# Kernel optimization log

Measured on AMD Instinct MI355X. Metric: run time of the kernel, lower is better.

The kernel has to match this reference:

```python
import jax, jax.numpy as jnp
import numpy as np

EPS = 1e-10
NUM_RELATION = 4
N_NODES = 50000
N_EDGES = 800000
D_IN = 128
D_H = 256


def rgc_layer(x, src, dst, rel, rel_w, rel_b, loop_w, loop_b):
    # torchdrug RelationalGraphConv: scatter-mean per (node, relation), then
    # linear over concatenated per-relation features + self-loop linear + relu.
    N, d = x.shape
    msg = x[src]                                      # [E, d] gather
    idx = dst * NUM_RELATION + rel                    # [E] bucket per (node, relation)
    num_seg = N * NUM_RELATION
    agg = jax.ops.segment_sum(msg, idx, num_segments=num_seg)            # [N*R, d]
    cnt = jax.ops.segment_sum(jnp.ones((msg.shape[0], 1), x.dtype), idx,
                              num_segments=num_seg)                       # [N*R, 1]
    update = (agg / (cnt + EPS)).reshape(N, NUM_RELATION * d)            # [N, R*d]
    out = update @ rel_w + rel_b + x @ loop_w + loop_b                   # [N, d_out]
    return jax.nn.relu(out)


def highway(x, hp_w, hp_b, ht_w, ht_b):
    proj = jax.nn.relu(x @ hp_w + hp_b)
    gate = jax.nn.sigmoid(x @ ht_w + ht_b)
    return gate * proj + (1.0 - gate) * x


def setup_inputs() -> dict:
    key = jax.random.key(0)
    ks = jax.random.split(key, 16)
    s = 0.02
    inp = {
        "x": jax.random.normal(ks[0], (N_NODES, D_IN), dtype=jnp.float32),
        "src": jax.random.randint(ks[1], (N_EDGES,), 0, N_NODES, dtype=jnp.int32),
        "dst": jax.random.randint(ks[2], (N_EDGES,), 0, N_NODES, dtype=jnp.int32),
        "rel": jax.random.randint(ks[3], (N_EDGES,), 0, NUM_RELATION, dtype=jnp.int32),
        # layer 1: RGC(128->256) + Highway(256)
        "rel_w1": jax.random.normal(ks[4], (NUM_RELATION * D_IN, D_H), dtype=jnp.float32) * s,
        "rel_b1": jnp.zeros((D_H,), jnp.float32),
        "loop_w1": jax.random.normal(ks[5], (D_IN, D_H), dtype=jnp.float32) * s,
        "loop_b1": jnp.zeros((D_H,), jnp.float32),
        "hp_w1": jax.random.normal(ks[6], (D_H, D_H), dtype=jnp.float32) * s,
        "hp_b1": jnp.zeros((D_H,), jnp.float32),
        "ht_w1": jax.random.normal(ks[7], (D_H, D_H), dtype=jnp.float32) * s,
        "ht_b1": jnp.full((D_H,), -2.0, jnp.float32),  # transform.bias.data.fill_(-2.0)
        # layer 2: RGC(256->256) + Highway(256)
        "rel_w2": jax.random.normal(ks[8], (NUM_RELATION * D_H, D_H), dtype=jnp.float32) * s,
        "rel_b2": jnp.zeros((D_H,), jnp.float32),
        "loop_w2": jax.random.normal(ks[9], (D_H, D_H), dtype=jnp.float32) * s,
        "loop_b2": jnp.zeros((D_H,), jnp.float32),
        "hp_w2": jax.random.normal(ks[10], (D_H, D_H), dtype=jnp.float32) * s,
        "hp_b2": jnp.zeros((D_H,), jnp.float32),
        "ht_w2": jax.random.normal(ks[11], (D_H, D_H), dtype=jnp.float32) * s,
        "ht_b2": jnp.full((D_H,), -2.0, jnp.float32),
    }
    return inp


def reference(x, src, dst, rel,
              rel_w1, rel_b1, loop_w1, loop_b1, hp_w1, hp_b1, ht_w1, ht_b1,
              rel_w2, rel_b2, loop_w2, loop_b2, hp_w2, hp_b2, ht_w2, ht_b2):
    h = rgc_layer(x, src, dst, rel, rel_w1, rel_b1, loop_w1, loop_b1)
    h = highway(h, hp_w1, hp_b1, ht_w1, ht_b1)
    h = rgc_layer(h, src, dst, rel, rel_w2, rel_b2, loop_w2, loop_b2)
    h = highway(h, hp_w2, hp_b2, ht_w2, ht_b2)
    return h  # node_feature, shape [N, 256]
```

## Files before the change

kernel.cpp:

```cpp
#include <hip/hip_runtime.h>

typedef __bf16 bf16_t;
typedef __bf16 bf16x8 __attribute__((ext_vector_type(8)));
typedef __bf16 bf16x4 __attribute__((ext_vector_type(4)));
typedef float f32x4 __attribute__((ext_vector_type(4)));
typedef int i32x4 __attribute__((ext_vector_type(4)));

#define BM 64

__device__ __forceinline__ void gload_lds16(const void* g, void* s) {
    __builtin_amdgcn_global_load_lds(
        (const __attribute__((address_space(1))) unsigned int*)g,
        (__attribute__((address_space(3))) unsigned int*)s, 16, 0, 0);
}

__device__ __forceinline__ void chunk_map(int g, int& row, int& kcol) {
    int L = g >> 3;
    int v = (g & 7) ^ (L & 7);
    row  = 2 * L + (v >> 2);
    kcol = (v & 3) << 3;
}

__device__ __forceinline__ int frag_off(int r, int quad) {
    int L = r >> 1;
    return L * 64 + (((((r & 1) << 2) | quad) ^ (L & 7)) << 3);
}

__global__ __launch_bounds__(256, 4) void gemm_k(
    const bf16_t* __restrict__ A, int lda, int M,
    const bf16_t* __restrict__ Bt, int K,
    const float* __restrict__ bias, int relu_flag,
    bf16_t* __restrict__ outb, int ldo, int ocol,
    int NTM)
{
    __shared__ __align__(16) bf16_t As[2][64 * 32];
    __shared__ __align__(16) bf16_t Bs[2][256 * 32];

    const int L   = blockIdx.x;
    const int xcd = L & 7;
    const int sup = L >> 3;
    const int mt  = sup * 8 + xcd;
    if (mt >= NTM) return;
    const int m0 = mt * BM;

    const int tid  = threadIdx.x;
    const int wave = tid >> 6, lane = tid & 63;
    const int wr   = wave >> 1, wc = wave & 1;
    const int lm   = lane & 15, quad = lane >> 4;

    const bf16_t* ag;
    const bf16_t* bg[4];
    {
        int row, kcol; chunk_map(tid, row, kcol);
        int gm = m0 + row; if (gm >= M) gm = M - 1;
        ag = A + (size_t)gm * lda + kcol;
    }
    #pragma unroll
    for (int j = 0; j < 4; j++) {
        int row, kcol; chunk_map(j * 256 + tid, row, kcol);
        bg[j] = Bt + (size_t)row * K + kcol;
    }

    f32x4 acc[2][8] = {};
    const int nt = K >> 5;

    gload_lds16(ag, &As[0][tid * 8]);
    #pragma unroll
    for (int j = 0; j < 4; j++)
        gload_lds16(bg[j], &Bs[0][(j * 256 + tid) * 8]);
    __syncthreads();

    int cur = 0;
    for (int t = 0; t < nt; ++t) {
        if (t + 1 < nt) {
            int k0n = (t + 1) << 5;
            gload_lds16(ag + k0n, &As[cur ^ 1][tid * 8]);
            #pragma unroll
            for (int j = 0; j < 4; j++)
                gload_lds16(bg[j] + k0n, &Bs[cur ^ 1][(j * 256 + tid) * 8]);
        }
        bf16x8 af[2];
        #pragma unroll
        for (int i = 0; i < 2; i++)
            af[i] = *(const bf16x8*)&As[cur][frag_off(wr * 32 + i * 16 + lm, quad)];
        #pragma unroll
        for (int ni = 0; ni < 8; ni++) {
            bf16x8 bfr = *(const bf16x8*)&Bs[cur][frag_off(wc * 128 + ni * 16 + lm, quad)];
            #pragma unroll
            for (int mi = 0; mi < 2; mi++)
                acc[mi][ni] = __builtin_amdgcn_mfma_f32_16x16x32_bf16(
                    af[mi], bfr, acc[mi][ni], 0, 0, 0);
        }
        __syncthreads();
        cur ^= 1;
    }

    #pragma unroll
    for (int mi = 0; mi < 2; mi++) {
        #pragma unroll
        for (int ni = 0; ni < 8; ni++) {
            int col = wc * 128 + ni * 16 + lm;
            float b = bias[col];
            #pragma unroll
            for (int r = 0; r < 4; r++) {
                int row = m0 + wr * 32 + mi * 16 + quad * 4 + r;
                if (row < M) {
                    float v = acc[mi][ni][r] + b;
                    if (relu_flag) v = fmaxf(v, 0.f);
                    outb[(size_t)row * ldo + ocol + col] = (bf16_t)v;
                }
            }
        }
    }
}

__global__ __launch_bounds__(256, 4) void gemm_hw2(
    const bf16_t* __restrict__ A, int M,
    const bf16_t* __restrict__ Bt,
    const float* __restrict__ bias,
    bf16_t* __restrict__ outb, int ldo, int ocol,
    float* __restrict__ outf, int NTM)
{
    __shared__ __align__(16) bf16_t As[2][64 * 32];
    __shared__ __align__(16) bf16_t Bs[2][256 * 32];

    const int L    = blockIdx.x;
    const int xcd  = L & 7;
    const int rest = L >> 3;
    const int nt2  = rest & 1;
    const int sup  = rest >> 1;
    const int mt   = sup * 8 + xcd;
    if (mt >= NTM) return;
    const int m0 = mt * BM;

    const int tid  = threadIdx.x;
    const int wave = tid >> 6, lane = tid & 63;
    const int lm   = lane & 15, quad = lane >> 4;

    const bf16_t* ag;
    const bf16_t* bg[4];
    {
        int row, kcol; chunk_map(tid, row, kcol);
        int gm = m0 + row; if (gm >= M) gm = M - 1;
        ag = A + (size_t)gm * 256 + kcol;
    }
    #pragma unroll
    for (int j = 0; j < 4; j++) {
        int row, kcol; chunk_map(j * 256 + tid, row, kcol);
        int grow = nt2 * 128 + row + ((row >= 128) ? 128 : 0);
        bg[j] = Bt + (size_t)grow * 256 + kcol;
    }

    f32x4 acc[16] = {};
    const int nt = 8;

    gload_lds16(ag, &As[0][tid * 8]);
    #pragma unroll
    for (int j = 0; j < 4; j++)
        gload_lds16(bg[j], &Bs[0][(j * 256 + tid) * 8]);
    __syncthreads();

    int cur = 0;
    for (int t = 0; t < nt; ++t) {
        if (t + 1 < nt) {
            int k0n = (t + 1) << 5;
            gload_lds16(ag + k0n, &As[cur ^ 1][tid * 8]);
            #pragma unroll
            for (int j = 0; j < 4; j++)
                gload_lds16(bg[j] + k0n, &Bs[cur ^ 1][(j * 256 + tid) * 8]);
        }
        bf16x8 af = *(const bf16x8*)&As[cur][frag_off(wave * 16 + lm, quad)];
        #pragma unroll
        for (int ni = 0; ni < 16; ni++) {
            bf16x8 bfr = *(const bf16x8*)&Bs[cur][frag_off(ni * 16 + lm, quad)];
            acc[ni] = __builtin_amdgcn_mfma_f32_16x16x32_bf16(
                af, bfr, acc[ni], 0, 0, 0);
        }
        __syncthreads();
        cur ^= 1;
    }

    #pragma unroll
    for (int ni = 0; ni < 8; ni++) {
        int col = nt2 * 128 + ni * 16 + lm;
        float bp  = bias[col];
        float bg2 = bias[256 + col];
        #pragma unroll
        for (int r = 0; r < 4; r++) {
            int row = m0 + wave * 16 + quad * 4 + r;
            if (row < M) {
                float p = acc[ni][r] + bp;
                float g = acc[ni + 8][r] + bg2;
                float s = 1.0f / (1.0f + __expf(-g));
                float hv = (float)A[(size_t)row * 256 + col];
                float v = s * fmaxf(p, 0.f) + (1.0f - s) * hv;
                if (outf) outf[(size_t)row * 256 + col] = v;
                else      outb[(size_t)row * ldo + ocol + col] = (bf16_t)v;
            }
        }
    }
}

__global__ void prep_all(
    const float* __restrict__ rel_w1, const float* __restrict__ loop_w1,
    const float* __restrict__ rel_w2, const float* __restrict__ loop_w2,
    const float* __restrict__ hp_w1,  const float* __restrict__ ht_w1,
    const float* __restrict__ hp_w2,  const float* __restrict__ ht_w2,
    bf16_t* __restrict__ W1t, bf16_t* __restrict__ W2t,
    bf16_t* __restrict__ Wh1t, bf16_t* __restrict__ Wh2t,
    const float* __restrict__ rb1, const float* __restrict__ lb1,
    const float* __restrict__ rb2, const float* __restrict__ lb2,
    const float* __restrict__ hpb1, const float* __restrict__ htb1,
    const float* __restrict__ hpb2, const float* __restrict__ htb2,
    float* __restrict__ bR1, float* __restrict__ bR2,
    float* __restrict__ bH1, float* __restrict__ bH2,
    const float* __restrict__ x, bf16_t* __restrict__ A1, int N,
    int* __restrict__ cnt, int NSEG, int cvb)
{
    __shared__ float sh[16][256];
    int b = blockIdx.x, tid = threadIdx.x;
    if (b < 184) {
        const float* W; bf16_t* Wt; int ldk, k0, n0, kb;
        if      (b < 32)  { W = rel_w1;  Wt = W1t;  ldk = 640;  k0 = 0;    n0 = 0;   kb = b; }
        else if (b < 40)  { W = loop_w1; Wt = W1t;  ldk = 640;  k0 = 512;  n0 = 0;   kb = b - 32; }
        else if (b < 104) { W = rel_w2;  Wt = W2t;  ldk = 1280; k0 = 0;    n0 = 0;   kb = b - 40; }
        else if (b < 120) { W = loop_w2; Wt = W2t;  ldk = 1280; k0 = 1024; n0 = 0;   kb = b - 104; }
        else if (b < 136) { W = hp_w1;   Wt = Wh1t; ldk = 256;  k0 = 0;    n0 = 0;   kb = b - 120; }
        else if (b < 152) { W = ht_w1;   Wt = Wh1t; ldk = 256;  k0 = 0;    n0 = 256; kb = b - 136; }
        else if (b < 168) { W = hp_w2;   Wt = Wh2t; ldk = 256;  k0 = 0;    n0 = 0;   kb = b - 152; }
        else              { W = ht_w2;   Wt = Wh2t; ldk = 256;  k0 = 0;    n0 = 256; kb = b - 168; }
        int kb16 = kb * 16;
        #pragma unroll
        for (int kk = 0; kk < 16; kk++)
            sh[kk][tid] = W[(size_t)(kb16 + kk) * 256 + tid];
        __syncthreads();
        bf16x8 o0, o1;
        #pragma unroll
        for (int j = 0; j < 8; j++) {
            o0[j] = (bf16_t)sh[j][tid];
            o1[j] = (bf16_t)sh[8 + j][tid];
        }
        bf16_t* p = Wt + (size_t)(n0 + tid) * ldk + k0 + kb16;
        *(bf16x8*)p = o0;
        *(bf16x8*)(p + 8) = o1;
    } else if (b == 184) {
        int t = tid;
        bR1[t] = rb1[t] + lb1[t];
        bR2[t] = rb2[t] + lb2[t];
        bH1[t] = hpb1[t]; bH1[256 + t] = htb1[t];
        bH2[t] = hpb2[t]; bH2[256 + t] = htb2[t];
    } else if (b < 185 + cvb) {
        int t = (b - 185) * 256 + tid;
        if (t < N * 32) {
            int row = t >> 5, c = (t & 31) << 2;
            f32x4 v = *(const f32x4*)(x + (size_t)row * 128 + c);
            bf16x4 o;
            o[0] = (bf16_t)v[0]; o[1] = (bf16_t)v[1]; o[2] = (bf16_t)v[2]; o[3] = (bf16_t)v[3];
            *(bf16x4*)(A1 + (size_t)row * 640 + 512 + c) = o;
        }
    } else {
        int t = ((b - 185 - cvb) * 256 + tid) * 4;
        if (t < NSEG) {
            i32x4 z = {0, 0, 0, 0};
            *(i32x4*)(cnt + t) = z;
        }
    }
}

__global__ void count_k(const int* __restrict__ dst, const int* __restrict__ rel,
                        int* __restrict__ cnt, int E)
{
    int e = blockIdx.x * blockDim.x + threadIdx.x;
    if (e < E) atomicAdd(&cnt[dst[e] * 4 + rel[e]], 1);
}

__global__ void scan_partial(const int* __restrict__ cnt, int* __restrict__ offs,
                             int* __restrict__ chunkSums, int NSEG)
{
    __shared__ int sh[256];
    int t = threadIdx.x;
    int idx = blockIdx.x * 256 + t;
    int v = (idx < NSEG) ? cnt[idx] : 0;
    sh[t] = v;
    __syncthreads();
    for (int d = 1; d < 256; d <<= 1) {
        int add = (t >= d) ? sh[t - d] : 0;
        __syncthreads();
        sh[t] += add;
        __syncthreads();
    }
    if (idx < NSEG) offs[idx] = sh[t] - v;
    if (t == 255) chunkSums[blockIdx.x] = sh[t];
}

__global__ void scan_chunks(int* __restrict__ chunkSums, int NCHUNK)
{
    __shared__ int sh[1024];
    int t = threadIdx.x;
    int v = (t < NCHUNK) ? chunkSums[t] : 0;
    sh[t] = v;
    __syncthreads();
    for (int d = 1; d < 1024; d <<= 1) {
        int add = (t >= d) ? sh[t - d] : 0;
        __syncthreads();
        sh[t] += add;
        __syncthreads();
    }
    if (t < NCHUNK) chunkSums[t] = sh[t] - v;
}

__global__ void scan_add(int* __restrict__ offs, const int* __restrict__ chunkSums,
                         int* __restrict__ cursor, int NSEG)
{
    int idx = blockIdx.x * 256 + threadIdx.x;
    if (idx < NSEG) {
        int o = offs[idx] + chunkSums[blockIdx.x];
        offs[idx] = o;
        cursor[idx] = o;
    }
}

__global__ void fill_k(const int* __restrict__ src, const int* __restrict__ dst,
                       const int* __restrict__ rel,
                       int* __restrict__ cursor, int* __restrict__ eidx, int E)
{
    int e = blockIdx.x * blockDim.x + threadIdx.x;
    if (e < E) {
        int seg = dst[e] * 4 + rel[e];
        int pos = atomicAdd(&cursor[seg], 1);
        eidx[pos] = src[e];
    }
}

__global__ void seg_mean256(const int* __restrict__ offs, const int* __restrict__ cnt,
                            const int* __restrict__ eidx,
                            const bf16_t* __restrict__ xb, int ldx,
                            bf16_t* __restrict__ Aout, int lda, int NSEG)
{
    int wv = (blockIdx.x << 2) + (threadIdx.x >> 6);
    if (wv >= NSEG) return;
    int lane = threadIdx.x & 63;
    int half = lane >> 5;
    int c = (lane & 31) << 3;
    int start = offs[wv];
    int n = cnt[wv];
    float acc[8] = {};
    int i = 0;
    for (; i + 8 <= n; i += 8) {
        int s0 = eidx[start + i + 0 + half];
        int s1 = eidx[start + i + 2 + half];
        int s2 = eidx[start + i + 4 + half];
        int s3 = eidx[start + i + 6 + half];
        bf16x8 v0 = *(const bf16x8*)(xb + (size_t)s0 * ldx + c);
        bf16x8 v1 = *(const bf16x8*)(xb + (size_t)s1 * ldx + c);
        bf16x8 v2 = *(const bf16x8*)(xb + (size_t)s2 * ldx + c);
        bf16x8 v3 = *(const bf16x8*)(xb + (size_t)s3 * ldx + c);
        #pragma unroll
        for (int j = 0; j < 8; j++)
            acc[j] += ((float)v0[j] + (float)v1[j]) + ((float)v2[j] + (float)v3[j]);
    }
    for (; i + 2 <= n; i += 2) {
        int s = eidx[start + i + half];
        bf16x8 v = *(const bf16x8*)(xb + (size_t)s * ldx + c);
        #pragma unroll
        for (int j = 0; j < 8; j++) acc[j] += (float)v[j];
    }
    if (i < n && half == 0) {
        int s = eidx[start + i];
        bf16x8 v = *(const bf16x8*)(xb + (size_t)s * ldx + c);
        #pragma unroll
        for (int j = 0; j < 8; j++) acc[j] += (float)v[j];
    }
    #pragma unroll
    for (int j = 0; j < 8; j++) acc[j] += __shfl_xor(acc[j], 32, 64);
    if (half == 0) {
        float inv = 1.0f / ((float)n + 1e-10f);
        int node = wv >> 2, r = wv & 3;
        bf16x8 o;
        #pragma unroll
        for (int j = 0; j < 8; j++) o[j] = (bf16_t)(acc[j] * inv);
        *(bf16x8*)(Aout + (size_t)node * lda + r * 256 + c) = o;
    }
}

__global__ void seg_mean128(const int* __restrict__ offs, const int* __restrict__ cnt,
                            const int* __restrict__ eidx,
                            const bf16_t* __restrict__ xb, int ldx,
                            bf16_t* __restrict__ Aout, int lda, int NSEG)
{
    int wv = (blockIdx.x << 2) + (threadIdx.x >> 6);
    if (wv >= NSEG) return;
    int lane = threadIdx.x & 63;
    int q = lane >> 4;
    int c = (lane & 15) << 3;
    int start = offs[wv];
    int n = cnt[wv];
    float acc[8] = {};
    int i = 0;
    for (; i + 8 <= n; i += 8) {
        int s0 = eidx[start + i + q];
        int s1 = eidx[start + i + 4 + q];
        bf16x8 v0 = *(const bf16x8*)(xb + (size_t)s0 * ldx + c);
        bf16x8 v1 = *(const bf16x8*)(xb + (size_t)s1 * ldx + c);
        #pragma unroll
        for (int j = 0; j < 8; j++) acc[j] += (float)v0[j] + (float)v1[j];
    }
    for (; i + 4 <= n; i += 4) {
        int s = eidx[start + i + q];
        bf16x8 v = *(const bf16x8*)(xb + (size_t)s * ldx + c);
        #pragma unroll
        for (int j = 0; j < 8; j++) acc[j] += (float)v[j];
    }
    if (q < n - i) {
        int s = eidx[start + i + q];
        bf16x8 v = *(const bf16x8*)(xb + (size_t)s * ldx + c);
        #pragma unroll
        for (int j = 0; j < 8; j++) acc[j] += (float)v[j];
    }
    #pragma unroll
    for (int j = 0; j < 8; j++) {
        acc[j] += __shfl_xor(acc[j], 16, 64);
        acc[j] += __shfl_xor(acc[j], 32, 64);
    }
    if (lane < 16) {
        float inv = 1.0f / ((float)n + 1e-10f);
        int node = wv >> 2, r = wv & 3;
        bf16x8 o;
        #pragma unroll
        for (int j = 0; j < 8; j++) o[j] = (bf16_t)(acc[j] * inv);
        *(bf16x8*)(Aout + (size_t)node * lda + r * 128 + c) = o;
    }
}

extern "C" void kernel_launch(void* const* d_in, const int* in_sizes, int n_in,
                              void* d_out, int out_size, void* d_ws, size_t ws_size,
                              hipStream_t stream)
{
    const float* x       = (const float*)d_in[0];
    const int*   src     = (const int*)d_in[1];
    const int*   dst     = (const int*)d_in[2];
    const int*   rel     = (const int*)d_in[3];
    const float* rel_w1  = (const float*)d_in[4];
    const float* rel_b1  = (const float*)d_in[5];
    const float* loop_w1 = (const float*)d_in[6];
    const float* loop_b1 = (const float*)d_in[7];
    const float* hp_w1   = (const float*)d_in[8];
    const float* hp_b1   = (const float*)d_in[9];
    const float* ht_w1   = (const float*)d_in[10];
    const float* ht_b1   = (const float*)d_in[11];
    const float* rel_w2  = (const float*)d_in[12];
    const float* rel_b2  = (const float*)d_in[13];
    const float* loop_w2 = (const float*)d_in[14];
    const float* loop_b2 = (const float*)d_in[15];
    const float* hp_w2   = (const float*)d_in[16];
    const float* hp_b2   = (const float*)d_in[17];
    const float* ht_w2   = (const float*)d_in[18];
    const float* ht_b2   = (const float*)d_in[19];

    const int N = in_sizes[0] / 128;
    const int E = in_sizes[1];
    const int NSEG = N * 4;
    const int NCHUNK = (NSEG + 255) / 256;
    float* out = (float*)d_out;

    char* ws = (char*)d_ws;
    size_t off = 0;
    auto alloc = [&](size_t bytes) {
        void* p = ws + off;
        off += (bytes + 255) & ~(size_t)255;
        return p;
    };
    int*    cnt    = (int*)alloc((size_t)NSEG * 4);
    int*    offs   = (int*)alloc((size_t)NSEG * 4);
    int*    cursor = (int*)alloc((size_t)NSEG * 4);
    int*    chunkS = (int*)alloc(4096);
    int*    eidx   = (int*)alloc((size_t)E * 4);
    bf16_t* A1     = (bf16_t*)alloc((size_t)N * 640 * 2);
    bf16_t* A2     = (bf16_t*)alloc((size_t)N * 1280 * 2);
    bf16_t* h      = (bf16_t*)alloc((size_t)N * 256 * 2);
    bf16_t* W1t    = (bf16_t*)alloc((size_t)256 * 640 * 2);
    bf16_t* W2t    = (bf16_t*)alloc((size_t)256 * 1280 * 2);
    bf16_t* Wh1t   = (bf16_t*)alloc((size_t)512 * 256 * 2);
    bf16_t* Wh2t   = (bf16_t*)alloc((size_t)512 * 256 * 2);
    float*  bR1    = (float*)alloc(256 * 4);
    float*  bR2    = (float*)alloc(256 * 4);
    float*  bH1    = (float*)alloc(512 * 4);
    float*  bH2    = (float*)alloc(512 * 4);

    dim3 blk(256);
    const int NTM = (N + BM - 1) / BM;
    const int supers = (NTM + 7) / 8;
    const int gridRGC = supers * 8;
    const int gridHW  = supers * 8 * 2;

    const int cvb = (N * 32 + 255) / 256;
    const int zb  = (NSEG / 4 + 255) / 256;
    prep_all<<<dim3(185 + cvb + zb), blk, 0, stream>>>(
        rel_w1, loop_w1, rel_w2, loop_w2, hp_w1, ht_w1, hp_w2, ht_w2,
        W1t, W2t, Wh1t, Wh2t,
        rel_b1, loop_b1, rel_b2, loop_b2, hp_b1, ht_b1, hp_b2, ht_b2,
        bR1, bR2, bH1, bH2,
        x, A1, N, cnt, NSEG, cvb);

    count_k<<<dim3((E + 255) / 256), blk, 0, stream>>>(dst, rel, cnt, E);
    scan_partial<<<dim3(NCHUNK), blk, 0, stream>>>(cnt, offs, chunkS, NSEG);
    scan_chunks<<<dim3(1), dim3(1024), 0, stream>>>(chunkS, NCHUNK);
    scan_add<<<dim3(NCHUNK), blk, 0, stream>>>(offs, chunkS, cursor, NSEG);
    fill_k<<<dim3((E + 255) / 256), blk, 0, stream>>>(src, dst, rel, cursor, eidx, E);

    seg_mean128<<<dim3((NSEG + 3) / 4), blk, 0, stream>>>(offs, cnt, eidx,
                                                          A1 + 512, 640, A1, 640, NSEG);
    gemm_k<<<dim3(gridRGC), blk, 0, stream>>>(A1, 640, N, W1t, 640,
                                              bR1, 1, h, 256, 0, NTM);
    gemm_hw2<<<dim3(gridHW), blk, 0, stream>>>(h, N, Wh1t, bH1,
                                               A2, 1280, 1024, nullptr, NTM);

    seg_mean256<<<dim3((NSEG + 3) / 4), blk, 0, stream>>>(offs, cnt, eidx,
                                                          A2 + 1024, 1280, A2, 1280, NSEG);
    gemm_k<<<dim3(gridRGC), blk, 0, stream>>>(A2, 1280, N, W2t, 1280,
                                              bR2, 1, h, 256, 0, NTM);
    gemm_hw2<<<dim3(gridHW), blk, 0, stream>>>(h, N, Wh2t, bH2,
                                               nullptr, 0, 0, out, NTM);
}
```

Measured before the change: 517.3 us.

## Fuse RGC linear and highway GEMMs into one kernel with LDS-resident hidden tile

Merges the relational GEMM and the highway GEMM into a single kernel per layer. The relu'd hidden tile stays in LDS and feeds the second GEMM directly, so the intermediate h buffer is never written to or re-read from global memory, and one launch per layer disappears. B operands are now loaded straight from global memory into registers rather than staged through LDS, double-buffered across k-steps. Occupancy hint drops from 4 to 3. Each block now does the full highway N dimension serially, giving half as many blocks for that stage, and the per-lane global weight loads rely on cache hits.

```diff
diff --git a/kernel.cpp b/kernel.cpp
--- a/kernel.cpp
+++ b/kernel.cpp
@@ -26,19 +26,28 @@
     return L * 64 + (((((r & 1) << 2) | quad) ^ (L & 7)) << 3);
 }
 
-__global__ __launch_bounds__(256, 4) void gemm_k(
-    const bf16_t* __restrict__ A, int lda, int M,
-    const bf16_t* __restrict__ Bt, int K,
-    const float* __restrict__ bias, int relu_flag,
+__device__ __forceinline__ int hs_off(int row, int col) {
+    int L = row >> 1;
+    int kin = col & 31;
+    return (col >> 5) * 2048 + L * 64 +
+           (((((row & 1) << 2) | (kin >> 3)) ^ (L & 7)) << 3) + (kin & 7);
+}
+
+__global__ __launch_bounds__(256, 3) void gemm_fused(
+    const bf16_t* __restrict__ A, int lda, int M, int K,
+    const bf16_t* __restrict__ Wt,
+    const float* __restrict__ bR,
+    const bf16_t* __restrict__ Wht,
+    const float* __restrict__ bH,
     bf16_t* __restrict__ outb, int ldo, int ocol,
-    int NTM)
+    float* __restrict__ outf, int NTM)
 {
     __shared__ __align__(16) bf16_t As[2][64 * 32];
-    __shared__ __align__(16) bf16_t Bs[2][256 * 32];
-
-    const int L   = blockIdx.x;
-    const int xcd = L & 7;
-    const int sup = L >> 3;
+    __shared__ __align__(16) bf16_t Hs[8 * 64 * 32];
+
+    const int Lb  = blockIdx.x;
+    const int xcd = Lb & 7;
+    const int sup = Lb >> 3;
     const int mt  = sup * 8 + xcd;
     if (mt >= NTM) return;
     const int m0 = mt * BM;
@@ -49,50 +58,61 @@
     const int lm   = lane & 15, quad = lane >> 4;
 
     const bf16_t* ag;
-    const bf16_t* bg[4];
     {
         int row, kcol; chunk_map(tid, row, kcol);
         int gm = m0 + row; if (gm >= M) gm = M - 1;
         ag = A + (size_t)gm * lda + kcol;
     }
+    const bf16_t* bbase = Wt + (size_t)(wc * 128 + lm) * K + quad * 8;
+
+    f32x4 acc1[2][8] = {};
+    const int nt = K >> 5;
+
+    bf16x8 b0[8], b1[8];
     #pragma unroll
-    for (int j = 0; j < 4; j++) {
-        int row, kcol; chunk_map(j * 256 + tid, row, kcol);
-        bg[j] = Bt + (size_t)row * K + kcol;
-    }
-
-    f32x4 acc[2][8] = {};
-    const int nt = K >> 5;
+    for (int ni = 0; ni < 8; ni++)
+        b0[ni] = *(const bf16x8*)(bbase + (size_t)ni * 16 * K);
 
     gload_lds16(ag, &As[0][tid * 8]);
-    #pragma unroll
-    for (int j = 0; j < 4; j++)
-        gload_lds16(bg[j], &Bs[0][(j * 256 + tid) * 8]);
     __syncthreads();
 
-    int cur = 0;
-    for (int t = 0; t < nt; ++t) {
-        if (t + 1 < nt) {
-            int k0n = (t + 1) << 5;
-            gload_lds16(ag + k0n, &As[cur ^ 1][tid * 8]);
-            #pragma unroll
-            for (int j = 0; j < 4; j++)
-                gload_lds16(bg[j] + k0n, &Bs[cur ^ 1][(j * 256 + tid) * 8]);
-        }
-        bf16x8 af[2];
-        #pragma unroll
-        for (int i = 0; i < 2; i++)
-            af[i] = *(const bf16x8*)&As[cur][frag_off(wr * 32 + i * 16 + lm, quad)];
-        #pragma unroll
-        for (int ni = 0; ni < 8; ni++) {
-            bf16x8 bfr = *(const bf16x8*)&Bs[cur][frag_off(wc * 128 + ni * 16 + lm, quad)];
-            #pragma unroll
-            for (int mi = 0; mi < 2; mi++)
-                acc[mi][ni] = __builtin_amdgcn_mfma_f32_16x16x32_bf16(
-                    af[mi], bfr, acc[mi][ni], 0, 0, 0);
-        }
-        __syncthreads();
-        cur ^= 1;
+    for (int t = 0; t < nt; t += 2) {
+        #pragma unroll
+        for (int ni = 0; ni < 8; ni++)
+            b1[ni] = *(const bf16x8*)(bbase + (size_t)ni * 16 * K + (t + 1) * 32);
+        gload_lds16(ag + (t + 1) * 32, &As[1][tid * 8]);
+        {
+            bf16x8 af[2];
+            #pragma unroll
+            for (int i = 0; i < 2; i++)
+                af[i] = *(const bf16x8*)&As[0][frag_off(wr * 32 + i * 16 + lm, quad)];
+            #pragma unroll
+            for (int ni = 0; ni < 8; ni++)
+                #pragma unroll
+                for (int mi = 0; mi < 2; mi++)
+                    acc1[mi][ni] = __builtin_amdgcn_mfma_f32_16x16x32_bf16(
+                        af[mi], b0[ni], acc1[mi][ni], 0, 0, 0);
+        }
+        __syncthreads();
+        if (t + 2 < nt) {
+            #pragma unroll
+            for (int ni = 0; ni < 8; ni++)
+                b0[ni] = *(const bf16x8*)(bbase + (size_t)ni * 16 * K + (t + 2) * 32);
+            gload_lds16(ag + (t + 2) * 32, &As[0][tid * 8]);
+        }
+        {
+            bf16x8 af[2];
+            #pragma unroll
+            for (int i = 0; i < 2; i++)
+                af[i] = *(const bf16x8*)&As[1][frag_off(wr * 32 + i * 16 + lm, quad)];
+            #pragma unroll
+            for (int ni = 0; ni < 8; ni++)
+                #pragma unroll
+                for (int mi = 0; mi < 2; mi++)
+                    acc1[mi][ni] = __builtin_amdgcn_mfma_f32_16x16x32_bf16(
+                        af[mi], b1[ni], acc1[mi][ni], 0, 0, 0);
+        }
+        __syncthreads();
     }
 
     #pragma unroll
@@ -100,102 +120,49 @@
         #pragma unroll
         for (int ni = 0; ni < 8; ni++) {
             int col = wc * 128 + ni * 16 + lm;
-            float b = bias[col];
+            float b = bR[col];
             #pragma unroll
             for (int r = 0; r < 4; r++) {
-                int row = m0 + wr * 32 + mi * 16 + quad * 4 + r;
-                if (row < M) {
-                    float v = acc[mi][ni][r] + b;
-                    if (relu_flag) v = fmaxf(v, 0.f);
-                    outb[(size_t)row * ldo + ocol + col] = (bf16_t)v;
+                int row = wr * 32 + mi * 16 + quad * 4 + r;
+                float v = fmaxf(acc1[mi][ni][r] + b, 0.f);
+                Hs[hs_off(row, col)] = (bf16_t)v;
+            }
+        }
+    }
+    __syncthreads();
+
+    #pragma unroll
+    for (int s = 0; s < 2; s++) {
+        f32x4 acc2[16] = {};
+        for (int t = 0; t < 8; t++) {
+            bf16x8 af2 = *(const bf16x8*)&Hs[t * 2048 + frag_off(wave * 16 + lm, quad)];
+            #pragma unroll
+            for (int ni = 0; ni < 16; ni++) {
+                int wrow = (ni < 8) ? (s * 128 + ni * 16 + lm)
+                                    : (256 + s * 128 + (ni - 8) * 16 + lm);
+                bf16x8 bfr = *(const bf16x8*)(Wht + (size_t)wrow * 256 + t * 32 + quad * 8);
+                acc2[ni] = __builtin_amdgcn_mfma_f32_16x16x32_bf16(
+                    af2, bfr, acc2[ni], 0, 0, 0);
+            }
+        }
+        #pragma unroll
+        for (int ni = 0; ni < 8; ni++) {
+            int col = s * 128 + ni * 16 + lm;
+            float bp  = bH[col];
+            float bg2 = bH[256 + col];
+            #pragma unroll
+            for (int r = 0; r < 4; r++) {
+                int row = wave * 16 + quad * 4 + r;
+                int grow = m0 + row;
+                if (grow < M) {
+                    float p = acc2[ni][r] + bp;
+                    float g = acc2[ni + 8][r] + bg2;
+                    float sg = 1.0f / (1.0f + __expf(-g));
+                    float hv = (float)Hs[hs_off(row, col)];
+                    float v = sg * fmaxf(p, 0.f) + (1.0f - sg) * hv;
+                    if (outf) outf[(size_t)grow * 256 + col] = v;
+                    else      outb[(size_t)grow * ldo + ocol + col] = (bf16_t)v;
                 }
-            }
-        }
-    }
-}
-
-__global__ __launch_bounds__(256, 4) void gemm_hw2(
-    const bf16_t* __restrict__ A, int M,
-    const bf16_t* __restrict__ Bt,
-    const float* __restrict__ bias,
-    bf16_t* __restrict__ outb, int ldo, int ocol,
-    float* __restrict__ outf, int NTM)
-{
-    __shared__ __align__(16) bf16_t As[2][64 * 32];
-    __shared__ __align__(16) bf16_t Bs[2][256 * 32];
-
-    const int L    = blockIdx.x;
-    const int xcd  = L & 7;
-    const int rest = L >> 3;
-    const int nt2  = rest & 1;
-    const int sup  = rest >> 1;
-    const int mt   = sup * 8 + xcd;
-    if (mt >= NTM) return;
-    const int m0 = mt * BM;
-
-    const int tid  = threadIdx.x;
-    const int wave = tid >> 6, lane = tid & 63;
-    const int lm   = lane & 15, quad = lane >> 4;
-
-    const bf16_t* ag;
-    const bf16_t* bg[4];
-    {
-        int row, kcol; chunk_map(tid, row, kcol);
-        int gm = m0 + row; if (gm >= M) gm = M - 1;
-        ag = A + (size_t)gm * 256 + kcol;
-    }
-    #pragma unroll
-    for (int j = 0; j < 4; j++) {
-        int row, kcol; chunk_map(j * 256 + tid, row, kcol);
-        int grow = nt2 * 128 + row + ((row >= 128) ? 128 : 0);
-        bg[j] = Bt + (size_t)grow * 256 + kcol;
-    }
-
-    f32x4 acc[16] = {};
-    const int nt = 8;
-
-    gload_lds16(ag, &As[0][tid * 8]);
-    #pragma unroll
-    for (int j = 0; j < 4; j++)
-        gload_lds16(bg[j], &Bs[0][(j * 256 + tid) * 8]);
-    __syncthreads();
-
-    int cur = 0;
-    for (int t = 0; t < nt; ++t) {
-        if (t + 1 < nt) {
-            int k0n = (t + 1) << 5;
-            gload_lds16(ag + k0n, &As[cur ^ 1][tid * 8]);
-            #pragma unroll
-            for (int j = 0; j < 4; j++)
-                gload_lds16(bg[j] + k0n, &Bs[cur ^ 1][(j * 256 + tid) * 8]);
-        }
-        bf16x8 af = *(const bf16x8*)&As[cur][frag_off(wave * 16 + lm, quad)];
-        #pragma unroll
-        for (int ni = 0; ni < 16; ni++) {
-            bf16x8 bfr = *(const bf16x8*)&Bs[cur][frag_off(ni * 16 + lm, quad)];
-            acc[ni] = __builtin_amdgcn_mfma_f32_16x16x32_bf16(
-                af, bfr, acc[ni], 0, 0, 0);
-        }
-        __syncthreads();
-        cur ^= 1;
-    }
-
-    #pragma unroll
-    for (int ni = 0; ni < 8; ni++) {
-        int col = nt2 * 128 + ni * 16 + lm;
-        float bp  = bias[col];
-        float bg2 = bias[256 + col];
-        #pragma unroll
-        for (int r = 0; r < 4; r++) {
-            int row = m0 + wave * 16 + quad * 4 + r;
-            if (row < M) {
-                float p = acc[ni][r] + bp;
-                float g = acc[ni + 8][r] + bg2;
-                float s = 1.0f / (1.0f + __expf(-g));
-                float hv = (float)A[(size_t)row * 256 + col];
-                float v = s * fmaxf(p, 0.f) + (1.0f - s) * hv;
-                if (outf) outf[(size_t)row * 256 + col] = v;
-                else      outb[(size_t)row * ldo + ocol + col] = (bf16_t)v;
             }
         }
     }
@@ -477,7 +444,6 @@
     int*    eidx   = (int*)alloc((size_t)E * 4);
     bf16_t* A1     = (bf16_t*)alloc((size_t)N * 640 * 2);
     bf16_t* A2     = (bf16_t*)alloc((size_t)N * 1280 * 2);
-    bf16_t* h      = (bf16_t*)alloc((size_t)N * 256 * 2);
     bf16_t* W1t    = (bf16_t*)alloc((size_t)256 * 640 * 2);
     bf16_t* W2t    = (bf16_t*)alloc((size_t)256 * 1280 * 2);
     bf16_t* Wh1t   = (bf16_t*)alloc((size_t)512 * 256 * 2);
@@ -490,8 +456,7 @@
     dim3 blk(256);
     const int NTM = (N + BM - 1) / BM;
     const int supers = (NTM + 7) / 8;
-    const int gridRGC = supers * 8;
-    const int gridHW  = supers * 8 * 2;
+    const int gridF = supers * 8;
 
     const int cvb = (N * 32 + 255) / 256;
     const int zb  = (NSEG / 4 + 255) / 256;
@@ -510,15 +475,13 @@
 
     seg_mean128<<<dim3((NSEG + 3) / 4), blk, 0, stream>>>(offs, cnt, eidx,
                                                           A1 + 512, 640, A1, 640, NSEG);
-    gemm_k<<<dim3(gridRGC), blk, 0, stream>>>(A1, 640, N, W1t, 640,
-                                              bR1, 1, h, 256, 0, NTM);
-    gemm_hw2<<<dim3(gridHW), blk, 0, stream>>>(h, N, Wh1t, bH1,
-                                               A2, 1280, 1024, nullptr, NTM);
+    gemm_fused<<<dim3(gridF), blk, 0, stream>>>(A1, 640, N, 640, W1t, bR1,
+                                                Wh1t, bH1,
+                                                A2, 1280, 1024, nullptr, NTM);
 
     seg_mean256<<<dim3((NSEG + 3) / 4), blk, 0, stream>>>(offs, cnt, eidx,
                                                           A2 + 1024, 1280, A2, 1280, NSEG);
-    gemm_k<<<dim3(gridRGC), blk, 0, stream>>>(A2, 1280, N, W2t, 1280,
-                                              bR2, 1, h, 256, 0, NTM);
-    gemm_hw2<<<dim3(gridHW), blk, 0, stream>>>(h, N, Wh2t, bH2,
-                                               nullptr, 0, 0, out, NTM);
-}
+    gemm_fused<<<dim3(gridF), blk, 0, stream>>>(A2, 1280, N, 1280, W2t, bR2,
+                                                Wh2t, bH2,
+                                                nullptr, 0, 0, out, NTM);
+}
```

After: 938.6 us. 1.81x slower.
